# Optimization experiments

Measured on AMD Instinct MI355X. Metric: run time of the kernel, lower is better.

The kernel has to match this reference:

```python
import jax, jax.numpy as jnp
import numpy as np


def silu(v):
    return v * jax.nn.sigmoid(v)


def setup_inputs() -> dict:
    key = jax.random.key(0)
    ks = jax.random.split(key, 12)
    B, L, Din, H, Dout = 8, 2048, 64, 256, 64
    d_model, d_state, d_conv, expand = 512, 16, 4, 2
    d_inner = expand * d_model
    dt_rank = d_model // 16  # ceil(512/16) = 32
    s = 0.02

    def n(k, shape):
        return jax.random.normal(k, shape, jnp.float32) * s

    return {
        "x": jax.random.normal(ks[0], (B, L, Din), jnp.float32),
        "enc_w1": n(ks[1], (H, Din)), "enc_b1": jnp.zeros((H,), jnp.float32),
        "enc_w2": n(ks[2], (d_model, H)), "enc_b2": jnp.zeros((d_model,), jnp.float32),
        "in_proj_w": n(ks[3], (2 * d_inner, d_model)),
        "conv_w": n(ks[4], (d_inner, 1, d_conv)), "conv_b": jnp.zeros((d_inner,), jnp.float32),
        "x_proj_w": n(ks[5], (dt_rank + 2 * d_state, d_inner)),
        "dt_proj_w": n(ks[6], (d_inner, dt_rank)), "dt_proj_b": jnp.zeros((d_inner,), jnp.float32),
        "A_log": jnp.log(jnp.broadcast_to(jnp.arange(1, d_state + 1, dtype=jnp.float32), (d_inner, d_state))),
        "D_param": jnp.ones((d_inner,), jnp.float32),
        "out_proj_w": n(ks[7], (d_model, d_inner)),
        "dec_w1": n(ks[8], (H, d_model)), "dec_b1": jnp.zeros((H,), jnp.float32),
        "dec_w2": n(ks[9], (Dout, H)), "dec_b2": jnp.zeros((Dout,), jnp.float32),
    }


def reference(x, enc_w1, enc_b1, enc_w2, enc_b2, in_proj_w, conv_w, conv_b,
              x_proj_w, dt_proj_w, dt_proj_b, A_log, D_param, out_proj_w,
              dec_w1, dec_b1, dec_w2, dec_b2):
    # ---- encoder MLP ----
    h = jax.nn.relu(x @ enc_w1.T + enc_b1)
    u = h @ enc_w2.T + enc_b2  # [B, L, d_model]
    B, L, _ = u.shape
    d_inner = in_proj_w.shape[0] // 2
    d_state = A_log.shape[1]
    dt_rank = dt_proj_w.shape[1]
    d_conv = conv_w.shape[-1]

    # ---- Mamba: input projection + gate split ----
    xz = u @ in_proj_w.T                       # [B, L, 2*d_inner]
    xm, z = jnp.split(xz, 2, axis=-1)

    # ---- causal depthwise conv1d ----
    xc = jnp.transpose(xm, (0, 2, 1))          # [B, d_inner, L]
    xc = jax.lax.conv_general_dilated(xc, conv_w, (1,), [(d_conv - 1, 0)],
                                      feature_group_count=d_inner)
    xc = xc + conv_b[None, :, None]
    xm = silu(jnp.transpose(xc, (0, 2, 1)))    # [B, L, d_inner]

    # ---- input-dependent SSM params ----
    dbl = xm @ x_proj_w.T                      # [B, L, dt_rank + 2*d_state]
    dt = dbl[..., :dt_rank]
    Bm = dbl[..., dt_rank:dt_rank + d_state]   # [B, L, d_state]
    Cm = dbl[..., dt_rank + d_state:]          # [B, L, d_state]
    delta = jax.nn.softplus(dt @ dt_proj_w.T + dt_proj_b)  # [B, L, d_inner]
    A = -jnp.exp(A_log)                        # [d_inner, d_state]

    # ---- selective scan over sequence ----
    def step(hs, inp):
        x_t, d_t, B_t, C_t = inp               # [B,d_inner],[B,d_inner],[B,d_state],[B,d_state]
        dA = jnp.exp(d_t[:, :, None] * A)      # [B, d_inner, d_state]
        hs = dA * hs + (d_t * x_t)[:, :, None] * B_t[:, None, :]
        y_t = jnp.einsum('bds,bs->bd', hs, C_t)
        return hs, y_t

    h0 = jnp.zeros((B, d_inner, d_state), xm.dtype)
    xs = (jnp.swapaxes(xm, 0, 1), jnp.swapaxes(delta, 0, 1),
          jnp.swapaxes(Bm, 0, 1), jnp.swapaxes(Cm, 0, 1))
    _, ys = jax.lax.scan(step, h0, xs)         # ys: [L, B, d_inner]

    y = jnp.swapaxes(ys, 0, 1) + xm * D_param  # skip term
    y = y * silu(z)                            # gate
    out = y @ out_proj_w.T                     # [B, L, d_model]

    # ---- decoder MLP ----
    h2 = jax.nn.relu(out @ dec_w1.T + dec_b1)
    return h2 @ dec_w2.T + dec_b2              # [B, L, output_dim]
```

## Files before the change

### kernel.cpp

```cpp
#include <hip/hip_runtime.h>
#include <hip/hip_bf16.h>

typedef __attribute__((ext_vector_type(8))) short bf16x8;
typedef __attribute__((ext_vector_type(4))) float f32x4;
typedef __attribute__((ext_vector_type(4))) unsigned short u16x4;
typedef __hip_bfloat16 bf16;

#define DEV __device__ __forceinline__
DEV float bf2f(bf16 v) { return __bfloat162float(v); }
DEV bf16  f2bf(float v) { return __float2bfloat16(v); }
DEV float sigmoidf_(float x) { return __builtin_amdgcn_rcpf(1.0f + __expf(-x)); }

typedef const __attribute__((address_space(1))) void* gptr_t;
typedef __attribute__((address_space(3))) void* lptr_t;

template<int N> DEV void waitcnt_vm() {
    if constexpr (N == 0) asm volatile("s_waitcnt vmcnt(0)" ::: "memory");
    else if constexpr (N == 2) asm volatile("s_waitcnt vmcnt(2)" ::: "memory");
    else if constexpr (N == 3) asm volatile("s_waitcnt vmcnt(3)" ::: "memory");
    else asm volatile("s_waitcnt vmcnt(4)" ::: "memory");
}

template<int BM, int BN, int ACT, int OUTBF>
__global__ __launch_bounds__(256)
void gemm_mfma(const bf16* __restrict__ A, int lda,
               const bf16* __restrict__ W, int ldw,
               const float* __restrict__ bias,
               void* __restrict__ Cp, int ldc, int K)
{
    constexpr int BK = 32;
    constexpr int WMS = BM / 2, WNS = BN / 2;
    constexpr int FM = WMS / 16, FN = WNS / 16;
    constexpr int AITER = (BM * BK) / (256 * 8);
    constexpr int BITER = (BN * BK) / (256 * 8);
    constexpr int NLD = AITER + BITER;
    constexpr int BUFB = (BM + BN) * BK * 2;

    __shared__ __align__(16) char smem[2 * BUFB];

    const int tid = threadIdx.x;
    const int lane = tid & 63;
    const int wid = tid >> 6;
    const int wm = wid >> 1, wn = wid & 1;
    const long m0 = (long)blockIdx.y * BM;
    const long n0 = (long)blockIdx.x * BN;

    f32x4 acc[FM][FN] = {};

    long aoff[AITER];
#pragma unroll
    for (int it = 0; it < AITER; ++it) {
        int q = it * 256 + tid;
        int r = q >> 2;
        aoff[it] = (long)(m0 + r) * lda * 2 + (((q & 3) * 16) ^ ((r & 3) << 4));
    }
    long boff[BITER];
#pragma unroll
    for (int it = 0; it < BITER; ++it) {
        int q = it * 256 + tid;
        int r = q >> 2;
        boff[it] = (long)(n0 + r) * ldw * 2 + (((q & 3) * 16) ^ ((r & 3) << 4));
    }

    const char* Ac = (const char*)A;
    const char* Wc = (const char*)W;

#pragma unroll
    for (int it = 0; it < AITER; ++it)
        __builtin_amdgcn_global_load_lds((gptr_t)(Ac + aoff[it]),
            (lptr_t)(smem + (it * 256 + wid * 64) * 16), 16, 0, 0);
#pragma unroll
    for (int it = 0; it < BITER; ++it)
        __builtin_amdgcn_global_load_lds((gptr_t)(Wc + boff[it]),
            (lptr_t)(smem + BM * BK * 2 + (it * 256 + wid * 64) * 16), 16, 0, 0);

    const int NK = K / BK;
    const int fr = lane & 15, fq = lane >> 4;
    const int swz = (fr & 3) << 4;
    int cur = 0;

    for (int ks = 0; ks < NK; ++ks) {
        if (ks + 1 < NK) {
            const long k2 = (long)(ks + 1) * BK * 2;
            char* dst = smem + (cur ^ 1) * BUFB;
#pragma unroll
            for (int it = 0; it < AITER; ++it)
                __builtin_amdgcn_global_load_lds((gptr_t)(Ac + aoff[it] + k2),
                    (lptr_t)(dst + (it * 256 + wid * 64) * 16), 16, 0, 0);
#pragma unroll
            for (int it = 0; it < BITER; ++it)
                __builtin_amdgcn_global_load_lds((gptr_t)(Wc + boff[it] + k2),
                    (lptr_t)(dst + BM * BK * 2 + (it * 256 + wid * 64) * 16), 16, 0, 0);
            waitcnt_vm<NLD>();
        } else {
            waitcnt_vm<0>();
        }
        __builtin_amdgcn_s_barrier();
        __builtin_amdgcn_sched_barrier(0);

        const char* base = smem + cur * BUFB;
        bf16x8 av[FM], bv[FN];
#pragma unroll
        for (int fm = 0; fm < FM; ++fm) {
            int ra = wm * WMS + fm * 16 + fr;
            av[fm] = *(const bf16x8*)(base + ra * 64 + ((fq * 16) ^ swz));
        }
#pragma unroll
        for (int fn = 0; fn < FN; ++fn) {
            int rb = wn * WNS + fn * 16 + fr;
            bv[fn] = *(const bf16x8*)(base + BM * BK * 2 + rb * 64 + ((fq * 16) ^ swz));
        }
#pragma unroll
        for (int fm = 0; fm < FM; ++fm)
#pragma unroll
            for (int fn = 0; fn < FN; ++fn)
                acc[fm][fn] = __builtin_amdgcn_mfma_f32_16x16x32_bf16(
                    av[fm], bv[fn], acc[fm][fn], 0, 0, 0);

        asm volatile("s_waitcnt lgkmcnt(0)" ::: "memory");
        __builtin_amdgcn_sched_barrier(0);
        __builtin_amdgcn_s_barrier();
        cur ^= 1;
    }

    float bcol[FN];
#pragma unroll
    for (int fn = 0; fn < FN; ++fn)
        bcol[fn] = bias ? bias[n0 + wn * WNS + fn * 16 + fr] : 0.0f;

    if constexpr (OUTBF) {
        constexpr int CST = BN + 8;
        bf16* ct = (bf16*)smem;
        for (int mh = 0; mh < BM / 64; ++mh) {
            __syncthreads();
            if (BM == 64 || wm == mh) {
#pragma unroll
                for (int fm = 0; fm < FM; ++fm) {
                    int lr0 = (BM == 64 ? wm * WMS : 0) + fm * 16 + fq * 4;
#pragma unroll
                    for (int fn = 0; fn < FN; ++fn) {
                        int lc = wn * WNS + fn * 16 + fr;
#pragma unroll
                        for (int r = 0; r < 4; ++r) {
                            float v = acc[fm][fn][r] + bcol[fn];
                            if (ACT == 1) v = fmaxf(v, 0.0f);
                            else if (ACT == 2)
                                v = fmaxf(v, 0.0f) + __logf(1.0f + __expf(-fabsf(v)));
                            else if (ACT == 3)
                                v = v * sigmoidf_(v);
                            ct[(lr0 + r) * CST + lc] = f2bf(v);
                        }
                    }
                }
            }
            __syncthreads();
            constexpr int GPR = BN / 8;
#pragma unroll
            for (int it = 0; it < (64 * GPR) / 256; ++it) {
                int idx = it * 256 + tid;
                int row = idx / GPR, cg = idx % GPR;
                bf16x8 v8 = *(const bf16x8*)&ct[row * CST + cg * 8];
                *(bf16x8*)((bf16*)Cp + (size_t)(m0 + mh * 64 + row) * ldc
                           + n0 + cg * 8) = v8;
            }
        }
    } else {
#pragma unroll
        for (int fn = 0; fn < FN; ++fn) {
            long col = n0 + wn * WNS + fn * 16 + fr;
#pragma unroll
            for (int fm = 0; fm < FM; ++fm) {
                long row0 = m0 + wm * WMS + fm * 16 + fq * 4;
#pragma unroll
                for (int r = 0; r < 4; ++r) {
                    float v = acc[fm][fn][r] + bcol[fn];
                    if (ACT == 1) v = fmaxf(v, 0.0f);
                    ((float*)Cp)[(size_t)(row0 + r) * ldc + col] = v;
                }
            }
        }
    }
}

struct CastJobs {
    const float* src[9];
    bf16* dst[9];
    int n[9];
};

__global__ __launch_bounds__(256)
void cast_bf16_kernel(CastJobs J)
{
    const int seg = blockIdx.y;
    const f32x4* s = (const f32x4*)J.src[seg];
    u16x4* d = (u16x4*)J.dst[seg];
    const int n4 = J.n[seg] >> 2;
    for (int i = blockIdx.x * 256 + threadIdx.x; i < n4; i += gridDim.x * 256) {
        f32x4 v = s[i];
        u16x4 o;
#pragma unroll
        for (int j = 0; j < 4; ++j) {
            bf16 b = f2bf(v[j]);
            o[j] = *(unsigned short*)&b;
        }
        d[i] = o;
    }
}

#define DSTATE 16
#define CHUNK 32

__global__ __launch_bounds__(256)
void conv_silu_kernel(const bf16* __restrict__ xmr, const float* __restrict__ cw,
                      const float* __restrict__ cb, bf16* __restrict__ xms, int L)
{
    const int NCc = L / 32;
    const int c = blockIdx.x % NCc;
    const int b = blockIdx.x / NCc;
    const int d = blockIdx.y * 256 + threadIdx.x;

    const float w0 = cw[d * 4 + 0], w1 = cw[d * 4 + 1];
    const float w2 = cw[d * 4 + 2], w3 = cw[d * 4 + 3];
    const float bb = cb[d];

    const int t0 = c * 32;
    float x0 = 0.f, x1 = 0.f, x2 = 0.f;
    if (t0 >= 3) {
        x0 = bf2f(xmr[(size_t)(b * L + t0 - 3) * 1024 + d]);
        x1 = bf2f(xmr[(size_t)(b * L + t0 - 2) * 1024 + d]);
        x2 = bf2f(xmr[(size_t)(b * L + t0 - 1) * 1024 + d]);
    }
    for (int t = t0; t < t0 + 32; ++t) {
        float x3 = bf2f(xmr[(size_t)(b * L + t) * 1024 + d]);
        float v = fmaf(w0, x0, fmaf(w1, x1, fmaf(w2, x2, fmaf(w3, x3, bb))));
        xms[(size_t)(b * L + t) * 1024 + d] = f2bf(v * sigmoidf_(v));
        x0 = x1; x1 = x2; x2 = x3;
    }
}

DEV bool load_A(const float* __restrict__ A_log, int d, float* As_)
{
    bool fastA = true;
#pragma unroll
    for (int s = 0; s < DSTATE; ++s) {
        As_[s] = -__expf(A_log[(size_t)d * DSTATE + s]);
        fastA = fastA && (fabsf(As_[s] + (float)(s + 1)) <= 1e-4f * (s + 1));
    }
    return fastA;
}

DEV void powa(float r, float* a)
{
    float r2 = r * r;
    float r3 = r2 * r;
    float r4 = r2 * r2;
    float r8 = r4 * r4;
    a[0] = r;       a[1] = r2;      a[2] = r3;      a[3] = r4;
    a[4] = r4 * r;  a[5] = r4 * r2; a[6] = r4 * r3; a[7] = r8;
    a[8] = r8 * r;  a[9] = r8 * r2; a[10] = r8 * r3; a[11] = r8 * r4;
    a[12] = a[11] * r; a[13] = a[11] * r2; a[14] = a[11] * r3; a[15] = r8 * r8;
}

__global__ __launch_bounds__(256)
void scan_pass1(const bf16* __restrict__ delta, bf16* xms ,
                const bf16* __restrict__ dblb, const float* __restrict__ A_log,
                const float* __restrict__ Dp,
                bf16* __restrict__ P, bf16* __restrict__ S, int L)
{
    const int NC = L / CHUNK;
    const int c = blockIdx.x % NC;
    const int b = blockIdx.x / NC;
    const int d = blockIdx.y * 256 + threadIdx.x;

    __shared__ float Bsh[CHUNK][DSTATE];
    __shared__ float Csh[CHUNK][DSTATE];
#pragma unroll
    for (int it = 0; it < CHUNK * DSTATE / 256; ++it) {
        int idx = threadIdx.x + it * 256;
        int t = idx >> 4, s = idx & 15;
        size_t base = (size_t)(b * L + c * CHUNK + t) * 64;
        Bsh[t][s] = bf2f(dblb[base + 32 + s]);
        Csh[t][s] = bf2f(dblb[base + 48 + s]);
    }
    __syncthreads();

    float As_[DSTATE];
    const bool fastA = load_A(A_log, d, As_);
    const float Dd = Dp[d];

    float h[DSTATE];
#pragma unroll
    for (int s = 0; s < DSTATE; ++s) h[s] = 0.f;

    const size_t rb = (size_t)(b * L + c * CHUNK);

    if (fastA) {
        float sumd = 0.f;
        for (int t = 0; t < CHUNK; ++t) {
            size_t g = (rb + t) * 1024 + d;
            float de = bf2f(delta[g]);
            float x  = bf2f(xms[g]);
            float dx = de * x;
            float r = __expf(-de);
            float a[DSTATE];
            powa(r, a);
            sumd += de;
            float yl = x * Dd;
#pragma unroll
            for (int s = 0; s < DSTATE; ++s) {
                h[s] = fmaf(a[s], h[s], dx * Bsh[t][s]);
                yl = fmaf(h[s], Csh[t][s], yl);
            }
            xms[g] = f2bf(yl);
        }
        float Rc = __expf(-sumd);
        float pa[DSTATE];
        powa(Rc, pa);
#pragma unroll
        for (int s = 0; s < DSTATE; ++s) {
            size_t o = ((size_t)(b * NC + c) * DSTATE + s) * 1024 + d;
            P[o] = f2bf(pa[s]);
            S[o] = f2bf(h[s]);
        }
    } else {
        float p[DSTATE];
#pragma unroll
        for (int s = 0; s < DSTATE; ++s) p[s] = 1.f;
        for (int t = 0; t < CHUNK; ++t) {
            size_t g = (rb + t) * 1024 + d;
            float de = bf2f(delta[g]);
            float x  = bf2f(xms[g]);
            float dx = de * x;
            float yl = x * Dd;
#pragma unroll
            for (int s = 0; s < DSTATE; ++s) {
                float dA = __expf(de * As_[s]);
                h[s] = fmaf(dA, h[s], dx * Bsh[t][s]);
                p[s] *= dA;
                yl = fmaf(h[s], Csh[t][s], yl);
            }
            xms[g] = f2bf(yl);
        }
#pragma unroll
        for (int s = 0; s < DSTATE; ++s) {
            size_t o = ((size_t)(b * NC + c) * DSTATE + s) * 1024 + d;
            P[o] = f2bf(p[s]);
            S[o] = f2bf(h[s]);
        }
    }
}

__global__ __launch_bounds__(256)
void scan_pass2(const bf16* P, const bf16* __restrict__ S, bf16* Hinit, int NC)
{
    int g = blockIdx.x * 256 + threadIdx.x;
    int d = g & 1023;
    int s = (g >> 10) & 15;
    int b = g >> 14;
    const size_t cs = (size_t)DSTATE * 1024;
    size_t o = ((size_t)(b * NC) * DSTATE + s) * 1024 + d;
    float h = 0.f;
    for (int c0 = 0; c0 < NC; c0 += 8) {
        float pv[8], sv[8];
#pragma unroll
        for (int j = 0; j < 8; ++j) {
            pv[j] = bf2f(P[o + j * cs]);
            sv[j] = bf2f(S[o + j * cs]);
        }
#pragma unroll
        for (int j = 0; j < 8; ++j) {
            Hinit[o + j * cs] = f2bf(h);
            h = fmaf(pv[j], h, sv[j]);
        }
        o += 8 * cs;
    }
}

__global__ __launch_bounds__(256)
void scan_pass3(const bf16* delta, const bf16* __restrict__ ylocal,
                const bf16* __restrict__ dblb, const float* __restrict__ A_log,
                const bf16* __restrict__ Hinit,
                const bf16* __restrict__ zs, bf16* Y, int L)
{
    const int NC = L / CHUNK;
    const int c = blockIdx.x % NC;
    const int b = blockIdx.x / NC;
    const int d = blockIdx.y * 256 + threadIdx.x;

    __shared__ float Csh[CHUNK][DSTATE];
#pragma unroll
    for (int it = 0; it < CHUNK * DSTATE / 256; ++it) {
        int idx = threadIdx.x + it * 256;
        int t = idx >> 4, s = idx & 15;
        Csh[t][s] = bf2f(dblb[(size_t)(b * L + c * CHUNK + t) * 64 + 48 + s]);
    }
    __syncthreads();

    float As_[DSTATE];
    const bool fastA = load_A(A_log, d, As_);

    float w[DSTATE];
#pragma unroll
    for (int s = 0; s < DSTATE; ++s)
        w[s] = bf2f(Hinit[((size_t)(b * NC + c) * DSTATE + s) * 1024 + d]);

    const size_t rb = (size_t)(b * L + c * CHUNK);

    if (fastA) {
        for (int t = 0; t < CHUNK; ++t) {
            size_t g = (rb + t) * 1024 + d;
            float de = bf2f(delta[g]);
            float yl = bf2f(ylocal[g]);
            float z  = bf2f(zs[g]);
            float r = __expf(-de);
            float a[DSTATE];
            powa(r, a);
            float c0 = 0.f, c1 = 0.f;
#pragma unroll
            for (int s = 0; s < DSTATE; s += 2) {
                w[s] *= a[s];
                c0 = fmaf(w[s], Csh[t][s], c0);
                w[s+1] *= a[s+1];
                c1 = fmaf(w[s+1], Csh[t][s+1], c1);
            }
            Y[g] = f2bf((yl + c0 + c1) * z);
        }
    } else {
        for (int t = 0; t < CHUNK; ++t) {
            size_t g = (rb + t) * 1024 + d;
            float de = bf2f(delta[g]);
            float yl = bf2f(ylocal[g]);
            float z  = bf2f(zs[g]);
            float c0 = 0.f, c1 = 0.f;
#pragma unroll
            for (int s = 0; s < DSTATE; s += 2) {
                w[s]   *= __expf(de * As_[s]);
                c0 = fmaf(w[s], Csh[t][s], c0);
                w[s+1] *= __expf(de * As_[s+1]);
                c1 = fmaf(w[s+1], Csh[t][s+1], c1);
            }
            Y[g] = f2bf((yl + c0 + c1) * z);
        }
    }
}


extern "C" void kernel_launch(void* const* d_in, const int* in_sizes, int n_in,
                              void* d_out, int out_size, void* d_ws, size_t ws_size,
                              hipStream_t stream)
{
    (void)in_sizes; (void)n_in; (void)out_size;

    const float* x         = (const float*)d_in[0];
    const float* enc_w1    = (const float*)d_in[1];
    const float* enc_b1    = (const float*)d_in[2];
    const float* enc_w2    = (const float*)d_in[3];
    const float* enc_b2    = (const float*)d_in[4];
    const float* in_proj_w = (const float*)d_in[5];
    const float* conv_w    = (const float*)d_in[6];
    const float* conv_b    = (const float*)d_in[7];
    const float* x_proj_w  = (const float*)d_in[8];
    const float* dt_proj_w = (const float*)d_in[9];
    const float* dt_proj_b = (const float*)d_in[10];
    const float* A_log     = (const float*)d_in[11];
    const float* D_param   = (const float*)d_in[12];
    const float* out_proj_w= (const float*)d_in[13];
    const float* dec_w1    = (const float*)d_in[14];
    const float* dec_b1    = (const float*)d_in[15];
    const float* dec_w2    = (const float*)d_in[16];
    const float* dec_b2    = (const float*)d_in[17];
    float* out = (float*)d_out;

    const int L = 2048, NC = L / CHUNK;

    bf16* wb = (bf16*)d_ws;
    size_t off = 0;
    bf16* w_enc1 = wb + off; off += 16384;
    bf16* w_enc2 = wb + off; off += 131072;
    bf16* w_inpj = wb + off; off += 1048576;
    bf16* w_xprj = wb + off; off += 65536;
    bf16* w_dtpj = wb + off; off += 32768;
    bf16* w_outp = wb + off; off += 524288;
    bf16* w_dec1 = wb + off; off += 131072;
    bf16* w_dec2 = wb + off; off += 16384;
    bf16* xbf    = wb + off; off += 1048576;
    const size_t fixedB = off * 2;

    const size_t PER_ROW = 9856;
    int SPLIT = 8;
    if      (fixedB + (size_t)16384 * PER_ROW <= ws_size) SPLIT = 1;
    else if (fixedB + (size_t) 8192 * PER_ROW <= ws_size) SPLIT = 2;
    else if (fixedB + (size_t) 4096 * PER_ROW <= ws_size) SPLIT = 4;

    const int NB = 8 / SPLIT;
    const int MR = NB * L;

    char* pb = (char*)d_ws + fixedB;
    bf16* hbf   = (bf16*)pb;
    bf16* ubf   = hbf   + (size_t)MR * 256;
    bf16* slot3 = ubf   + (size_t)MR * 512;
    bf16* zbf   = slot3 + (size_t)MR * 1024;
    bf16* xms   = zbf   + (size_t)MR * 1024;
    bf16* dblb  = xms   + (size_t)MR * 1024;
    bf16* Pb    = dblb  + (size_t)MR * 64;
    bf16* Sb    = Pb    + (size_t)MR * 512;

    CastJobs J;
    J.src[0] = enc_w1;     J.dst[0] = w_enc1; J.n[0] = 16384;
    J.src[1] = enc_w2;     J.dst[1] = w_enc2; J.n[1] = 131072;
    J.src[2] = in_proj_w;  J.dst[2] = w_inpj; J.n[2] = 1048576;
    J.src[3] = x_proj_w;   J.dst[3] = w_xprj; J.n[3] = 65536;
    J.src[4] = dt_proj_w;  J.dst[4] = w_dtpj; J.n[4] = 32768;
    J.src[5] = out_proj_w; J.dst[5] = w_outp; J.n[5] = 524288;
    J.src[6] = dec_w1;     J.dst[6] = w_dec1; J.n[6] = 131072;
    J.src[7] = dec_w2;     J.dst[7] = w_dec2; J.n[7] = 16384;
    J.src[8] = x;          J.dst[8] = xbf;    J.n[8] = 1048576;
    cast_bf16_kernel<<<dim3(128, 9), 256, 0, stream>>>(J);

    dim3 blk(256);
    for (int p = 0; p < SPLIT; ++p) {
        const bf16* xp  = xbf + (size_t)p * MR * 64;
        float*     outp = out + (size_t)p * MR * 64;

        gemm_mfma<64,128,1,1><<<dim3(2, MR/64), blk, 0, stream>>>(
            xp, 64, w_enc1, 64, enc_b1, hbf, 256, 64);
        gemm_mfma<128,128,0,1><<<dim3(4, MR/128), blk, 0, stream>>>(
            hbf, 256, w_enc2, 256, enc_b2, ubf, 512, 256);
        gemm_mfma<128,128,0,1><<<dim3(8, MR/128), blk, 0, stream>>>(
            ubf, 512, w_inpj, 512, nullptr, slot3, 1024, 512);
        gemm_mfma<128,128,3,1><<<dim3(8, MR/128), blk, 0, stream>>>(
            ubf, 512, w_inpj + (size_t)1024 * 512, 512, nullptr, zbf, 1024, 512);
        conv_silu_kernel<<<dim3(NB * (L/32), 4), blk, 0, stream>>>(
            slot3, conv_w, conv_b, xms, L);
        gemm_mfma<64,64,0,1><<<dim3(1, MR/64), blk, 0, stream>>>(
            xms, 1024, w_xprj, 1024, nullptr, dblb, 64, 1024);
        gemm_mfma<128,128,2,1><<<dim3(8, MR/128), blk, 0, stream>>>(
            dblb, 64, w_dtpj, 32, dt_proj_b, slot3, 1024, 32);
        scan_pass1<<<dim3(NB * NC, 4), blk, 0, stream>>>(
            slot3, xms, dblb, A_log, D_param, Pb, Sb, L);
        scan_pass2<<<dim3(NB * 64), blk, 0, stream>>>(Pb, Sb, Pb, NC);
        scan_pass3<<<dim3(NB * NC, 4), blk, 0, stream>>>(
            slot3, xms, dblb, A_log, Pb, zbf, slot3 , L);
        gemm_mfma<128,128,0,1><<<dim3(4, MR/128), blk, 0, stream>>>(
            slot3, 1024, w_outp, 1024, nullptr, ubf, 512, 1024);
        gemm_mfma<64,128,1,1><<<dim3(2, MR/64), blk, 0, stream>>>(
            ubf, 512, w_dec1, 512, dec_b1, hbf, 256, 512);
        gemm_mfma<64,64,0,0><<<dim3(1, MR/64), blk, 0, stream>>>(
            hbf, 256, w_dec2, 256, dec_b2, outp, 64, 256);
    }
}
```

Before: 349.8 us.

## Halve scan chunk size and process two channels per thread with packed bf16 access

The chunked selective scan now uses 16-step chunks instead of 32, doubling the number of chunks, and each thread handles two adjacent d_inner channels using 32-bit packed bf16 loads and stores. The fast-A check is split from A loading so A values are only loaded on the slow path. Shorter chunks shorten the serial dependency per thread while two-channel packing widens memory accesses and adds ILP. In exchange the P/S carry buffers double in size and the serial pass2 over chunks gets twice as long, with more per-thread registers.

```diff
diff --git a/kernel.cpp b/kernel.cpp
--- a/kernel.cpp
+++ b/kernel.cpp
@@ -10,6 +10,16 @@
 DEV float bf2f(bf16 v) { return __bfloat162float(v); }
 DEV bf16  f2bf(float v) { return __float2bfloat16(v); }
 DEV float sigmoidf_(float x) { return __builtin_amdgcn_rcpf(1.0f + __expf(-x)); }
+
+DEV void unpk(unsigned int v, float& lo, float& hi) {
+    lo = __uint_as_float(v << 16);
+    hi = __uint_as_float(v & 0xffff0000u);
+}
+DEV unsigned int pk(float lo, float hi) {
+    bf16 a = f2bf(lo), b = f2bf(hi);
+    return (unsigned int)*(unsigned short*)&a |
+           ((unsigned int)*(unsigned short*)&b << 16);
+}
 
 typedef const __attribute__((address_space(1))) void* gptr_t;
 typedef __attribute__((address_space(3))) void* lptr_t;
@@ -208,7 +218,7 @@
 }
 
 #define DSTATE 16
-#define CHUNK 32
+#define CHUNK 16
 
 __global__ __launch_bounds__(256)
 void conv_silu_kernel(const bf16* __restrict__ xmr, const float* __restrict__ cw,
@@ -238,15 +248,22 @@
     }
 }
 
-DEV bool load_A(const float* __restrict__ A_log, int d, float* As_)
-{
-    bool fastA = true;
+DEV bool chk_A(const float* __restrict__ A_log, int d)
+{
+    bool f = true;
 #pragma unroll
     for (int s = 0; s < DSTATE; ++s) {
+        float v = -__expf(A_log[(size_t)d * DSTATE + s]);
+        f = f && (fabsf(v + (float)(s + 1)) <= 1e-4f * (s + 1));
+    }
+    return f;
+}
+
+DEV void load_A(const float* __restrict__ A_log, int d, float* As_)
+{
+#pragma unroll
+    for (int s = 0; s < DSTATE; ++s)
         As_[s] = -__expf(A_log[(size_t)d * DSTATE + s]);
-        fastA = fastA && (fabsf(As_[s] + (float)(s + 1)) <= 1e-4f * (s + 1));
-    }
-    return fastA;
 }
 
 DEV void powa(float r, float* a)
@@ -262,7 +279,7 @@
 }
 
 __global__ __launch_bounds__(256)
-void scan_pass1(const bf16* __restrict__ delta, bf16* xms ,
+void scan_pass1(const bf16* __restrict__ delta, bf16* xms,
                 const bf16* __restrict__ dblb, const float* __restrict__ A_log,
                 const float* __restrict__ Dp,
                 bf16* __restrict__ P, bf16* __restrict__ S, int L)
@@ -270,82 +287,90 @@
     const int NC = L / CHUNK;
     const int c = blockIdx.x % NC;
     const int b = blockIdx.x / NC;
-    const int d = blockIdx.y * 256 + threadIdx.x;
+    const int d0 = blockIdx.y * 512 + threadIdx.x * 2;
 
     __shared__ float Bsh[CHUNK][DSTATE];
     __shared__ float Csh[CHUNK][DSTATE];
-#pragma unroll
-    for (int it = 0; it < CHUNK * DSTATE / 256; ++it) {
-        int idx = threadIdx.x + it * 256;
-        int t = idx >> 4, s = idx & 15;
+    {
+        int t = threadIdx.x >> 4, s = threadIdx.x & 15;
         size_t base = (size_t)(b * L + c * CHUNK + t) * 64;
         Bsh[t][s] = bf2f(dblb[base + 32 + s]);
         Csh[t][s] = bf2f(dblb[base + 48 + s]);
     }
     __syncthreads();
 
-    float As_[DSTATE];
-    const bool fastA = load_A(A_log, d, As_);
-    const float Dd = Dp[d];
-
-    float h[DSTATE];
-#pragma unroll
-    for (int s = 0; s < DSTATE; ++s) h[s] = 0.f;
+    const bool fastA = chk_A(A_log, d0) && chk_A(A_log, d0 + 1);
+    const float Dd0 = Dp[d0], Dd1 = Dp[d0 + 1];
+
+    float h0[DSTATE], h1[DSTATE];
+#pragma unroll
+    for (int s = 0; s < DSTATE; ++s) { h0[s] = 0.f; h1[s] = 0.f; }
 
     const size_t rb = (size_t)(b * L + c * CHUNK);
 
     if (fastA) {
-        float sumd = 0.f;
+        float sum0 = 0.f, sum1 = 0.f;
         for (int t = 0; t < CHUNK; ++t) {
-            size_t g = (rb + t) * 1024 + d;
-            float de = bf2f(delta[g]);
-            float x  = bf2f(xms[g]);
-            float dx = de * x;
-            float r = __expf(-de);
-            float a[DSTATE];
-            powa(r, a);
-            sumd += de;
-            float yl = x * Dd;
+            size_t g = (rb + t) * 1024 + d0;
+            float de0, de1, x0, x1;
+            unpk(*(const unsigned int*)&delta[g], de0, de1);
+            unpk(*(const unsigned int*)&xms[g], x0, x1);
+            float dx0 = de0 * x0, dx1 = de1 * x1;
+            float a0[DSTATE], a1[DSTATE];
+            powa(__expf(-de0), a0);
+            powa(__expf(-de1), a1);
+            sum0 += de0; sum1 += de1;
+            float y0 = x0 * Dd0, y1 = x1 * Dd1;
 #pragma unroll
             for (int s = 0; s < DSTATE; ++s) {
-                h[s] = fmaf(a[s], h[s], dx * Bsh[t][s]);
-                yl = fmaf(h[s], Csh[t][s], yl);
-            }
-            xms[g] = f2bf(yl);
-        }
-        float Rc = __expf(-sumd);
-        float pa[DSTATE];
-        powa(Rc, pa);
+                h0[s] = fmaf(a0[s], h0[s], dx0 * Bsh[t][s]);
+                y0 = fmaf(h0[s], Csh[t][s], y0);
+                h1[s] = fmaf(a1[s], h1[s], dx1 * Bsh[t][s]);
+                y1 = fmaf(h1[s], Csh[t][s], y1);
+            }
+            *(unsigned int*)&xms[g] = pk(y0, y1);
+        }
+        float pa0[DSTATE], pa1[DSTATE];
+        powa(__expf(-sum0), pa0);
+        powa(__expf(-sum1), pa1);
 #pragma unroll
         for (int s = 0; s < DSTATE; ++s) {
-            size_t o = ((size_t)(b * NC + c) * DSTATE + s) * 1024 + d;
-            P[o] = f2bf(pa[s]);
-            S[o] = f2bf(h[s]);
+            size_t o = ((size_t)(b * NC + c) * DSTATE + s) * 1024 + d0;
+            *(unsigned int*)&P[o] = pk(pa0[s], pa1[s]);
+            *(unsigned int*)&S[o] = pk(h0[s], h1[s]);
         }
     } else {
-        float p[DSTATE];
-#pragma unroll
-        for (int s = 0; s < DSTATE; ++s) p[s] = 1.f;
+        float As0[DSTATE], As1[DSTATE];
+        load_A(A_log, d0, As0);
+        load_A(A_log, d0 + 1, As1);
+        float p0[DSTATE], p1[DSTATE];
+#pragma unroll
+        for (int s = 0; s < DSTATE; ++s) { p0[s] = 1.f; p1[s] = 1.f; }
         for (int t = 0; t < CHUNK; ++t) {
-            size_t g = (rb + t) * 1024 + d;
-            float de = bf2f(delta[g]);
-            float x  = bf2f(xms[g]);
-            float dx = de * x;
-            float yl = x * Dd;
+            size_t g = (rb + t) * 1024 + d0;
+            float de0, de1, x0, x1;
+            unpk(*(const unsigned int*)&delta[g], de0, de1);
+            unpk(*(const unsigned int*)&xms[g], x0, x1);
+            float dx0 = de0 * x0, dx1 = de1 * x1;
+            float y0 = x0 * Dd0, y1 = x1 * Dd1;
 #pragma unroll
             for (int s = 0; s < DSTATE; ++s) {
-                float dA = __expf(de * As_[s]);
-                h[s] = fmaf(dA, h[s], dx * Bsh[t][s]);
-                p[s] *= dA;
-                yl = fmaf(h[s], Csh[t][s], yl);
-            }
-            xms[g] = f2bf(yl);
+                float dA0 = __expf(de0 * As0[s]);
+                float dA1 = __expf(de1 * As1[s]);
+                h0[s] = fmaf(dA0, h0[s], dx0 * Bsh[t][s]);
+                p0[s] *= dA0;
+                y0 = fmaf(h0[s], Csh[t][s], y0);
+                h1[s] = fmaf(dA1, h1[s], dx1 * Bsh[t][s]);
+                p1[s] *= dA1;
+                y1 = fmaf(h1[s], Csh[t][s], y1);
+            }
+            *(unsigned int*)&xms[g] = pk(y0, y1);
         }
 #pragma unroll
         for (int s = 0; s < DSTATE; ++s) {
-            size_t o = ((size_t)(b * NC + c) * DSTATE + s) * 1024 + d;
-            P[o] = f2bf(p[s]);
-            S[o] = f2bf(h[s]);
+            size_t o = ((size_t)(b * NC + c) * DSTATE + s) * 1024 + d0;
+            *(unsigned int*)&P[o] = pk(p0[s], p1[s]);
+            *(unsigned int*)&S[o] = pk(h0[s], h1[s]);
         }
     }
 }
@@ -354,92 +379,102 @@
 void scan_pass2(const bf16* P, const bf16* __restrict__ S, bf16* Hinit, int NC)
 {
     int g = blockIdx.x * 256 + threadIdx.x;
-    int d = g & 1023;
-    int s = (g >> 10) & 15;
-    int b = g >> 14;
+    int dp = (g & 511) * 2;
+    int s = (g >> 9) & 15;
+    int b = g >> 13;
     const size_t cs = (size_t)DSTATE * 1024;
-    size_t o = ((size_t)(b * NC) * DSTATE + s) * 1024 + d;
-    float h = 0.f;
+    size_t o = ((size_t)(b * NC) * DSTATE + s) * 1024 + dp;
+    float h0 = 0.f, h1 = 0.f;
     for (int c0 = 0; c0 < NC; c0 += 8) {
-        float pv[8], sv[8];
+        float pv0[8], pv1[8], sv0[8], sv1[8];
 #pragma unroll
         for (int j = 0; j < 8; ++j) {
-            pv[j] = bf2f(P[o + j * cs]);
-            sv[j] = bf2f(S[o + j * cs]);
+            unpk(*(const unsigned int*)&P[o + j * cs], pv0[j], pv1[j]);
+            unpk(*(const unsigned int*)&S[o + j * cs], sv0[j], sv1[j]);
         }
 #pragma unroll
         for (int j = 0; j < 8; ++j) {
-            Hinit[o + j * cs] = f2bf(h);
-            h = fmaf(pv[j], h, sv[j]);
+            *(unsigned int*)&Hinit[o + j * cs] = pk(h0, h1);
+            h0 = fmaf(pv0[j], h0, sv0[j]);
+            h1 = fmaf(pv1[j], h1, sv1[j]);
         }
         o += 8 * cs;
     }
 }
 
 __global__ __launch_bounds__(256)
-void scan_pass3(const bf16* delta, const bf16* __restrict__ ylocal,
+void scan_pass3(bf16* dY, const bf16* __restrict__ ylocal,
                 const bf16* __restrict__ dblb, const float* __restrict__ A_log,
                 const bf16* __restrict__ Hinit,
-                const bf16* __restrict__ zs, bf16* Y, int L)
+                const bf16* __restrict__ zs, int L)
 {
     const int NC = L / CHUNK;
     const int c = blockIdx.x % NC;
     const int b = blockIdx.x / NC;
-    const int d = blockIdx.y * 256 + threadIdx.x;
+    const int d0 = blockIdx.y * 512 + threadIdx.x * 2;
 
     __shared__ float Csh[CHUNK][DSTATE];
-#pragma unroll
-    for (int it = 0; it < CHUNK * DSTATE / 256; ++it) {
-        int idx = threadIdx.x + it * 256;
-        int t = idx >> 4, s = idx & 15;
+    {
+        int t = threadIdx.x >> 4, s = threadIdx.x & 15;
         Csh[t][s] = bf2f(dblb[(size_t)(b * L + c * CHUNK + t) * 64 + 48 + s]);
     }
     __syncthreads();
 
-    float As_[DSTATE];
-    const bool fastA = load_A(A_log, d, As_);
-
-    float w[DSTATE];
-#pragma unroll
-    for (int s = 0; s < DSTATE; ++s)
-        w[s] = bf2f(Hinit[((size_t)(b * NC + c) * DSTATE + s) * 1024 + d]);
+    const bool fastA = chk_A(A_log, d0) && chk_A(A_log, d0 + 1);
+
+    float w0[DSTATE], w1[DSTATE];
+#pragma unroll
+    for (int s = 0; s < DSTATE; ++s) {
+        size_t o = ((size_t)(b * NC + c) * DSTATE + s) * 1024 + d0;
+        unpk(*(const unsigned int*)&Hinit[o], w0[s], w1[s]);
+    }
 
     const size_t rb = (size_t)(b * L + c * CHUNK);
 
     if (fastA) {
         for (int t = 0; t < CHUNK; ++t) {
-            size_t g = (rb + t) * 1024 + d;
-            float de = bf2f(delta[g]);
-            float yl = bf2f(ylocal[g]);
-            float z  = bf2f(zs[g]);
-            float r = __expf(-de);
-            float a[DSTATE];
-            powa(r, a);
-            float c0 = 0.f, c1 = 0.f;
+            size_t g = (rb + t) * 1024 + d0;
+            float de0, de1, yl0, yl1, z0, z1;
+            unpk(*(const unsigned int*)&dY[g], de0, de1);
+            unpk(*(const unsigned int*)&ylocal[g], yl0, yl1);
+            unpk(*(const unsigned int*)&zs[g], z0, z1);
+            float a0[DSTATE], a1[DSTATE];
+            powa(__expf(-de0), a0);
+            powa(__expf(-de1), a1);
+            float c00 = 0.f, c01 = 0.f, c10 = 0.f, c11 = 0.f;
 #pragma unroll
             for (int s = 0; s < DSTATE; s += 2) {
-                w[s] *= a[s];
-                c0 = fmaf(w[s], Csh[t][s], c0);
-                w[s+1] *= a[s+1];
-                c1 = fmaf(w[s+1], Csh[t][s+1], c1);
-            }
-            Y[g] = f2bf((yl + c0 + c1) * z);
+                w0[s] *= a0[s];
+                c00 = fmaf(w0[s], Csh[t][s], c00);
+                w0[s+1] *= a0[s+1];
+                c01 = fmaf(w0[s+1], Csh[t][s+1], c01);
+                w1[s] *= a1[s];
+                c10 = fmaf(w1[s], Csh[t][s], c10);
+                w1[s+1] *= a1[s+1];
+                c11 = fmaf(w1[s+1], Csh[t][s+1], c11);
+            }
+            *(unsigned int*)&dY[g] =
+                pk((yl0 + c00 + c01) * z0, (yl1 + c10 + c11) * z1);
         }
     } else {
+        float As0[DSTATE], As1[DSTATE];
+        load_A(A_log, d0, As0);
+        load_A(A_log, d0 + 1, As1);
         for (int t = 0; t < CHUNK; ++t) {
-            size_t g = (rb + t) * 1024 + d;
-            float de = bf2f(delta[g]);
-            float yl = bf2f(ylocal[g]);
-            float z  = bf2f(zs[g]);
-            float c0 = 0.f, c1 = 0.f;
-#pragma unroll
-            for (int s = 0; s < DSTATE; s += 2) {
-                w[s]   *= __expf(de * As_[s]);
-                c0 = fmaf(w[s], Csh[t][s], c0);
-                w[s+1] *= __expf(de * As_[s+1]);
-                c1 = fmaf(w[s+1], Csh[t][s+1], c1);
-            }
-            Y[g] = f2bf((yl + c0 + c1) * z);
+            size_t g = (rb + t) * 1024 + d0;
+            float de0, de1, yl0, yl1, z0, z1;
+            unpk(*(const unsigned int*)&dY[g], de0, de1);
+            unpk(*(const unsigned int*)&ylocal[g], yl0, yl1);
+            unpk(*(const unsigned int*)&zs[g], z0, z1);
+            float c00 = 0.f, c10 = 0.f;
+#pragma unroll
+            for (int s = 0; s < DSTATE; ++s) {
+                w0[s] *= __expf(de0 * As0[s]);
+                c00 = fmaf(w0[s], Csh[t][s], c00);
+                w1[s] *= __expf(de1 * As1[s]);
+                c10 = fmaf(w1[s], Csh[t][s], c10);
+            }
+            *(unsigned int*)&dY[g] = pk((yl0 + c00) * z0, (yl1 + c10) * z1);
         }
     }
 }
@@ -486,7 +521,7 @@
     bf16* xbf    = wb + off; off += 1048576;
     const size_t fixedB = off * 2;
 
-    const size_t PER_ROW = 9856;
+    const size_t PER_ROW = 11904;
     int SPLIT = 8;
     if      (fixedB + (size_t)16384 * PER_ROW <= ws_size) SPLIT = 1;
     else if (fixedB + (size_t) 8192 * PER_ROW <= ws_size) SPLIT = 2;
@@ -503,7 +538,7 @@
     bf16* xms   = zbf   + (size_t)MR * 1024;
     bf16* dblb  = xms   + (size_t)MR * 1024;
     bf16* Pb    = dblb  + (size_t)MR * 64;
-    bf16* Sb    = Pb    + (size_t)MR * 512;
+    bf16* Sb    = Pb    + (size_t)MR * 1024;
 
     CastJobs J;
     J.src[0] = enc_w1;     J.dst[0] = w_enc1; J.n[0] = 16384;
@@ -536,11 +571,11 @@
             xms, 1024, w_xprj, 1024, nullptr, dblb, 64, 1024);
         gemm_mfma<128,128,2,1><<<dim3(8, MR/128), blk, 0, stream>>>(
             dblb, 64, w_dtpj, 32, dt_proj_b, slot3, 1024, 32);
-        scan_pass1<<<dim3(NB * NC, 4), blk, 0, stream>>>(
+        scan_pass1<<<dim3(NB * NC, 2), blk, 0, stream>>>(
             slot3, xms, dblb, A_log, D_param, Pb, Sb, L);
-        scan_pass2<<<dim3(NB * 64), blk, 0, stream>>>(Pb, Sb, Pb, NC);
-        scan_pass3<<<dim3(NB * NC, 4), blk, 0, stream>>>(
-            slot3, xms, dblb, A_log, Pb, zbf, slot3 , L);
+        scan_pass2<<<dim3(NB * 32), blk, 0, stream>>>(Pb, Sb, Pb, NC);
+        scan_pass3<<<dim3(NB * NC, 2), blk, 0, stream>>>(
+            slot3, xms, dblb, A_log, Pb, zbf, L);
         gemm_mfma<128,128,0,1><<<dim3(4, MR/128), blk, 0, stream>>>(
             slot3, 1024, w_outp, 1024, nullptr, ubf, 512, 1024);
         gemm_mfma<64,128,1,1><<<dim3(2, MR/64), blk, 0, stream>>>(
```

Result: slower. 377.9 us (+8.0%).

## Fuse dt_proj+softplus into scan pass1 and merge in_proj x/z GEMMs

Applied to the files above, without the earlier changes.

Moves the dt_proj GEMM and softplus into scan_pass1, where each thread computes delta from the 32-wide dt slice held in shared memory and its own weight row, then writes delta out for pass3. The two in_proj GEMM launches become one dual-output launch that applies SiLU only to the z half. Pass3 gets a 4-way accumulator split. This removes two launches and one full delta write and read pass, at the cost of extra scalar FMA work in pass1 plus 32 weight registers per thread.

```diff
diff --git a/kernel.cpp b/kernel.cpp
--- a/kernel.cpp
+++ b/kernel.cpp
@@ -21,12 +21,20 @@
     else asm volatile("s_waitcnt vmcnt(4)" ::: "memory");
 }
 
-template<int BM, int BN, int ACT, int OUTBF>
+template<int A> DEV float actf(float v) {
+    if constexpr (A == 1) return fmaxf(v, 0.0f);
+    else if constexpr (A == 2) return fmaxf(v, 0.0f) + __logf(1.0f + __expf(-fabsf(v)));
+    else if constexpr (A == 3) return v * sigmoidf_(v);
+    else return v;
+}
+
+template<int BM, int BN, int ACT, int OUTBF, int DUAL, int ACT2>
 __global__ __launch_bounds__(256)
 void gemm_mfma(const bf16* __restrict__ A, int lda,
                const bf16* __restrict__ W, int ldw,
                const float* __restrict__ bias,
-               void* __restrict__ Cp, int ldc, int K)
+               void* __restrict__ Cp, void* __restrict__ Cp2, int NH,
+               int ldc, int K)
 {
     constexpr int BK = 32;
     constexpr int WMS = BM / 2, WNS = BN / 2;
@@ -128,6 +136,11 @@
     for (int fn = 0; fn < FN; ++fn)
         bcol[fn] = bias ? bias[n0 + wn * WNS + fn * 16 + fr] : 0.0f;
 
+    void* dstP = Cp;
+    long nb0 = n0;
+    bool use2 = false;
+    if (DUAL && n0 >= NH) { dstP = Cp2; nb0 = n0 - NH; use2 = true; }
+
     if constexpr (OUTBF) {
         constexpr int CST = BN + 8;
         bf16* ct = (bf16*)smem;
@@ -143,11 +156,7 @@
 #pragma unroll
                         for (int r = 0; r < 4; ++r) {
                             float v = acc[fm][fn][r] + bcol[fn];
-                            if (ACT == 1) v = fmaxf(v, 0.0f);
-                            else if (ACT == 2)
-                                v = fmaxf(v, 0.0f) + __logf(1.0f + __expf(-fabsf(v)));
-                            else if (ACT == 3)
-                                v = v * sigmoidf_(v);
+                            v = (DUAL && use2) ? actf<ACT2>(v) : actf<ACT>(v);
                             ct[(lr0 + r) * CST + lc] = f2bf(v);
                         }
                     }
@@ -160,8 +169,8 @@
                 int idx = it * 256 + tid;
                 int row = idx / GPR, cg = idx % GPR;
                 bf16x8 v8 = *(const bf16x8*)&ct[row * CST + cg * 8];
-                *(bf16x8*)((bf16*)Cp + (size_t)(m0 + mh * 64 + row) * ldc
-                           + n0 + cg * 8) = v8;
+                *(bf16x8*)((bf16*)dstP + (size_t)(m0 + mh * 64 + row) * ldc
+                           + nb0 + cg * 8) = v8;
             }
         }
     } else {
@@ -174,7 +183,7 @@
 #pragma unroll
                 for (int r = 0; r < 4; ++r) {
                     float v = acc[fm][fn][r] + bcol[fn];
-                    if (ACT == 1) v = fmaxf(v, 0.0f);
+                    v = actf<ACT>(v);
                     ((float*)Cp)[(size_t)(row0 + r) * ldc + col] = v;
                 }
             }
@@ -262,9 +271,10 @@
 }
 
 __global__ __launch_bounds__(256)
-void scan_pass1(const bf16* __restrict__ delta, bf16* xms ,
-                const bf16* __restrict__ dblb, const float* __restrict__ A_log,
-                const float* __restrict__ Dp,
+void scan_pass1(bf16* __restrict__ delta_out, bf16* xms,
+                const bf16* __restrict__ dblb,
+                const bf16* __restrict__ wdt, const float* __restrict__ dtb,
+                const float* __restrict__ A_log, const float* __restrict__ Dp,
                 bf16* __restrict__ P, bf16* __restrict__ S, int L)
 {
     const int NC = L / CHUNK;
@@ -274,6 +284,7 @@
 
     __shared__ float Bsh[CHUNK][DSTATE];
     __shared__ float Csh[CHUNK][DSTATE];
+    __shared__ float Tsh[CHUNK][33];
 #pragma unroll
     for (int it = 0; it < CHUNK * DSTATE / 256; ++it) {
         int idx = threadIdx.x + it * 256;
@@ -282,7 +293,29 @@
         Bsh[t][s] = bf2f(dblb[base + 32 + s]);
         Csh[t][s] = bf2f(dblb[base + 48 + s]);
     }
+#pragma unroll
+    for (int it = 0; it < CHUNK * 32 / 256; ++it) {
+        int idx = threadIdx.x + it * 256;
+        int t = idx >> 5, k = idx & 31;
+        Tsh[t][k] = bf2f(dblb[(size_t)(b * L + c * CHUNK + t) * 64 + k]);
+    }
     __syncthreads();
+
+    float wd[32];
+    {
+        bf16x8 wv[4];
+#pragma unroll
+        for (int j = 0; j < 4; ++j)
+            wv[j] = *(const bf16x8*)&wdt[(size_t)d * 32 + j * 8];
+#pragma unroll
+        for (int j = 0; j < 4; ++j)
+#pragma unroll
+            for (int e = 0; e < 8; ++e) {
+                short sv = wv[j][e];
+                wd[j * 8 + e] = bf2f(*(bf16*)&sv);
+            }
+    }
+    const float bias_d = dtb[d];
 
     float As_[DSTATE];
     const bool fastA = load_A(A_log, d, As_);
@@ -298,7 +331,20 @@
         float sumd = 0.f;
         for (int t = 0; t < CHUNK; ++t) {
             size_t g = (rb + t) * 1024 + d;
-            float de = bf2f(delta[g]);
+            float v0 = 0.f, v1 = 0.f, v2 = 0.f, v3 = 0.f;
+#pragma unroll
+            for (int k = 0; k < 32; k += 4) {
+                v0 = fmaf(Tsh[t][k],     wd[k],     v0);
+                v1 = fmaf(Tsh[t][k + 1], wd[k + 1], v1);
+                v2 = fmaf(Tsh[t][k + 2], wd[k + 2], v2);
+                v3 = fmaf(Tsh[t][k + 3], wd[k + 3], v3);
+            }
+            float v = (v0 + v1) + (v2 + v3) + bias_d;
+            float sp = fmaxf(v, 0.0f) + __logf(1.0f + __expf(-fabsf(v)));
+            bf16 dbf = f2bf(sp);
+            delta_out[g] = dbf;
+            float de = bf2f(dbf);
+
             float x  = bf2f(xms[g]);
             float dx = de * x;
             float r = __expf(-de);
@@ -328,7 +374,18 @@
         for (int s = 0; s < DSTATE; ++s) p[s] = 1.f;
         for (int t = 0; t < CHUNK; ++t) {
             size_t g = (rb + t) * 1024 + d;
-            float de = bf2f(delta[g]);
+            float v0 = 0.f, v1 = 0.f;
+#pragma unroll
+            for (int k = 0; k < 32; k += 2) {
+                v0 = fmaf(Tsh[t][k],     wd[k],     v0);
+                v1 = fmaf(Tsh[t][k + 1], wd[k + 1], v1);
+            }
+            float v = v0 + v1 + bias_d;
+            float sp = fmaxf(v, 0.0f) + __logf(1.0f + __expf(-fabsf(v)));
+            bf16 dbf = f2bf(sp);
+            delta_out[g] = dbf;
+            float de = bf2f(dbf);
+
             float x  = bf2f(xms[g]);
             float dx = de * x;
             float yl = x * Dd;
@@ -377,10 +434,10 @@
 }
 
 __global__ __launch_bounds__(256)
-void scan_pass3(const bf16* delta, const bf16* __restrict__ ylocal,
+void scan_pass3(bf16* dY, const bf16* __restrict__ ylocal,
                 const bf16* __restrict__ dblb, const float* __restrict__ A_log,
                 const bf16* __restrict__ Hinit,
-                const bf16* __restrict__ zs, bf16* Y, int L)
+                const bf16* __restrict__ zs, int L)
 {
     const int NC = L / CHUNK;
     const int c = blockIdx.x % NC;
@@ -409,26 +466,30 @@
     if (fastA) {
         for (int t = 0; t < CHUNK; ++t) {
             size_t g = (rb + t) * 1024 + d;
-            float de = bf2f(delta[g]);
+            float de = bf2f(dY[g]);
             float yl = bf2f(ylocal[g]);
             float z  = bf2f(zs[g]);
             float r = __expf(-de);
             float a[DSTATE];
             powa(r, a);
-            float c0 = 0.f, c1 = 0.f;
-#pragma unroll
-            for (int s = 0; s < DSTATE; s += 2) {
+            float c0 = 0.f, c1 = 0.f, c2 = 0.f, c3 = 0.f;
+#pragma unroll
+            for (int s = 0; s < DSTATE; s += 4) {
                 w[s] *= a[s];
                 c0 = fmaf(w[s], Csh[t][s], c0);
                 w[s+1] *= a[s+1];
                 c1 = fmaf(w[s+1], Csh[t][s+1], c1);
-            }
-            Y[g] = f2bf((yl + c0 + c1) * z);
+                w[s+2] *= a[s+2];
+                c2 = fmaf(w[s+2], Csh[t][s+2], c2);
+                w[s+3] *= a[s+3];
+                c3 = fmaf(w[s+3], Csh[t][s+3], c3);
+            }
+            dY[g] = f2bf((yl + (c0 + c1) + (c2 + c3)) * z);
         }
     } else {
         for (int t = 0; t < CHUNK; ++t) {
             size_t g = (rb + t) * 1024 + d;
-            float de = bf2f(delta[g]);
+            float de = bf2f(dY[g]);
             float yl = bf2f(ylocal[g]);
             float z  = bf2f(zs[g]);
             float c0 = 0.f, c1 = 0.f;
@@ -439,7 +500,7 @@
                 w[s+1] *= __expf(de * As_[s+1]);
                 c1 = fmaf(w[s+1], Csh[t][s+1], c1);
             }
-            Y[g] = f2bf((yl + c0 + c1) * z);
+            dY[g] = f2bf((yl + c0 + c1) * z);
         }
     }
 }
@@ -522,30 +583,26 @@
         const bf16* xp  = xbf + (size_t)p * MR * 64;
         float*     outp = out + (size_t)p * MR * 64;
 
-        gemm_mfma<64,128,1,1><<<dim3(2, MR/64), blk, 0, stream>>>(
-            xp, 64, w_enc1, 64, enc_b1, hbf, 256, 64);
-        gemm_mfma<128,128,0,1><<<dim3(4, MR/128), blk, 0, stream>>>(
-            hbf, 256, w_enc2, 256, enc_b2, ubf, 512, 256);
-        gemm_mfma<128,128,0,1><<<dim3(8, MR/128), blk, 0, stream>>>(
-            ubf, 512, w_inpj, 512, nullptr, slot3, 1024, 512);
-        gemm_mfma<128,128,3,1><<<dim3(8, MR/128), blk, 0, stream>>>(
-            ubf, 512, w_inpj + (size_t)1024 * 512, 512, nullptr, zbf, 1024, 512);
+        gemm_mfma<64,128,1,1,0,0><<<dim3(2, MR/64), blk, 0, stream>>>(
+            xp, 64, w_enc1, 64, enc_b1, hbf, nullptr, 0, 256, 64);
+        gemm_mfma<128,128,0,1,0,0><<<dim3(4, MR/128), blk, 0, stream>>>(
+            hbf, 256, w_enc2, 256, enc_b2, ubf, nullptr, 0, 512, 256);
+        gemm_mfma<128,128,0,1,1,3><<<dim3(16, MR/128), blk, 0, stream>>>(
+            ubf, 512, w_inpj, 512, nullptr, slot3, zbf, 1024, 1024, 512);
         conv_silu_kernel<<<dim3(NB * (L/32), 4), blk, 0, stream>>>(
             slot3, conv_w, conv_b, xms, L);
-        gemm_mfma<64,64,0,1><<<dim3(1, MR/64), blk, 0, stream>>>(
-            xms, 1024, w_xprj, 1024, nullptr, dblb, 64, 1024);
-        gemm_mfma<128,128,2,1><<<dim3(8, MR/128), blk, 0, stream>>>(
-            dblb, 64, w_dtpj, 32, dt_proj_b, slot3, 1024, 32);
+        gemm_mfma<64,64,0,1,0,0><<<dim3(1, MR/64), blk, 0, stream>>>(
+            xms, 1024, w_xprj, 1024, nullptr, dblb, nullptr, 0, 64, 1024);
         scan_pass1<<<dim3(NB * NC, 4), blk, 0, stream>>>(
-            slot3, xms, dblb, A_log, D_param, Pb, Sb, L);
+            slot3, xms, dblb, w_dtpj, dt_proj_b, A_log, D_param, Pb, Sb, L);
         scan_pass2<<<dim3(NB * 64), blk, 0, stream>>>(Pb, Sb, Pb, NC);
         scan_pass3<<<dim3(NB * NC, 4), blk, 0, stream>>>(
-            slot3, xms, dblb, A_log, Pb, zbf, slot3 , L);
-        gemm_mfma<128,128,0,1><<<dim3(4, MR/128), blk, 0, stream>>>(
-            slot3, 1024, w_outp, 1024, nullptr, ubf, 512, 1024);
-        gemm_mfma<64,128,1,1><<<dim3(2, MR/64), blk, 0, stream>>>(
-            ubf, 512, w_dec1, 512, dec_b1, hbf, 256, 512);
-        gemm_mfma<64,64,0,0><<<dim3(1, MR/64), blk, 0, stream>>>(
-            hbf, 256, w_dec2, 256, dec_b2, outp, 64, 256);
-    }
-}
+            slot3, xms, dblb, A_log, Pb, zbf, L);
+        gemm_mfma<128,128,0,1,0,0><<<dim3(4, MR/128), blk, 0, stream>>>(
+            slot3, 1024, w_outp, 1024, nullptr, ubf, nullptr, 0, 512, 1024);
+        gemm_mfma<64,128,1,1,0,0><<<dim3(2, MR/64), blk, 0, stream>>>(
+            ubf, 512, w_dec1, 512, dec_b1, hbf, nullptr, 0, 256, 512);
+        gemm_mfma<64,64,0,0,0,0><<<dim3(1, MR/64), blk, 0, stream>>>(
+            hbf, 256, w_dec2, 256, dec_b2, outp, nullptr, 0, 64, 256);
+    }
+}
```

Measured after the change: 371.5 us. 1.06x slower.
